# Kernel optimization log

Measured on AMD Instinct MI355X. Metric: run time of the kernel, lower is better.

The kernel has to match this reference:

```python
import jax, jax.numpy as jnp
import numpy as np

N = 100000   # nodes (single ntype)
E = 1600000  # edges per relation
R = 3        # relations
IN, H, OUT = 128, 128, 64


def setup_inputs() -> dict:
    key = jax.random.key(0)
    ks = jax.random.split(key, 6)
    x = jax.random.normal(ks[0], (N, IN), jnp.float32)
    W1 = jax.random.normal(ks[1], (R, IN, H), jnp.float32) * 0.05
    b1 = jax.random.normal(ks[2], (R, H), jnp.float32) * 0.05
    W2 = jax.random.normal(ks[3], (R, H, OUT), jnp.float32) * 0.05
    b2 = jax.random.normal(ks[4], (R, OUT), jnp.float32) * 0.05
    # edge_index[l, r, 0] = src ids, edge_index[l, r, 1] = dst ids for layer l, relation r
    edge_index = jax.random.randint(ks[5], (2, R, 2, E), 0, N, jnp.int32)
    return {"x": x, "W1": W1, "b1": b1, "W2": W2, "b2": b2, "edge_index": edge_index}


def _graph_conv(h, src, dst, W, b, n):
    """DGL GraphConv with norm='both': D_dst^{-1/2} A D_src^{-1/2} h W + b.
    Degrees are clamped to min 1 as in DGL."""
    ones = jnp.ones(src.shape[0], h.dtype)
    deg_out = jnp.clip(jax.ops.segment_sum(ones, src, num_segments=n), 1.0)
    deg_in = jnp.clip(jax.ops.segment_sum(ones, dst, num_segments=n), 1.0)
    m = (h * jax.lax.rsqrt(deg_out)[:, None])[src]          # [E, d] gather
    agg = jax.ops.segment_sum(m, dst, num_segments=n)       # [N, d] scatter-add
    return (agg * jax.lax.rsqrt(deg_in)[:, None]) @ W + b


def _hetero_layer(h, edges, W, b):
    # HeteroGraphConv default aggregate='sum' over relations sharing a dst ntype
    n = h.shape[0]
    out = _graph_conv(h, edges[0, 0], edges[0, 1], W[0], b[0], n)
    for r in range(1, edges.shape[0]):
        out = out + _graph_conv(h, edges[r, 0], edges[r, 1], W[r], b[r], n)
    return out


def reference(x, W1, b1, W2, b2, edge_index):
    h = jax.nn.relu(_hetero_layer(x, edge_index[0], W1, b1))  # dropout = identity (eval)
    return _hetero_layer(h, edge_index[1], W2, b2)
```

## Files before the change

kernel.cpp:

```cpp
#include <hip/hip_runtime.h>

#define N_NODES 100000
#define N_EDGES 1600000
#define NBUCK 250
#define BSZ 400
#define CHUNK 8192
#define NCHUNK 196
#define CAP 8192
#define MTILES 6250
#define NTILE 13
#define NKEY (BSZ * NTILE)
#define NKEYP 5376

typedef _Float16 half8 __attribute__((ext_vector_type(8)));
typedef _Float16 half2v __attribute__((ext_vector_type(2)));
typedef float floatx4 __attribute__((ext_vector_type(4)));

#define OFF_DEG   0ull
#define OFF_GC    4800000ull
#define OFF_BB    4806144ull
#define OFF_BC    4812288ull
#define OFF_RS    4818432ull
#define OFF_START 9618432ull
#define OFF_PAIRS 12018432ull
#define OFF_XH    50418432ull
#define OFF_W1F   76018432ull
#define OFF_W2F   76116736ull
#define OFF_AGG   76165888ull
#define OFF_HW    152965888ull

#define OFF_DDS   OFF_AGG
#define OFF_GCS   (OFF_AGG + 19200000ull)
#define OFF_BBS   (OFF_AGG + 19206144ull)
#define OFF_BCS   (OFF_AGG + 19212288ull)

__device__ __forceinline__ void lds_scan256(int* a) {
    int t = threadIdx.x;
    for (int off = 1; off < 256; off <<= 1) {
        int v = (t >= off) ? a[t - off] : 0;
        __syncthreads();
        a[t] += v;
        __syncthreads();
    }
}

__global__ __launch_bounds__(256) void k_bhist2(const int* __restrict__ ei,
                                                int* __restrict__ gcount_d,
                                                int* __restrict__ gcount_s) {
    int lr = blockIdx.y;
    int e0 = blockIdx.x * CHUNK;
    int n = min(CHUNK, N_EDGES - e0);
    const int* bs = ei + (size_t)lr * 2 * N_EDGES + e0;
    const int* bd = bs + N_EDGES;
    __shared__ int lhs[256];
    __shared__ int lhd[256];
    int t = threadIdx.x;
    lhs[t] = 0; lhd[t] = 0;
    __syncthreads();
    for (int i = t; i < n; i += 256) {
        atomicAdd(&lhs[bs[i] / BSZ], 1);
        atomicAdd(&lhd[bd[i] / BSZ], 1);
    }
    __syncthreads();
    if (t < NBUCK) {
        if (lhd[t]) atomicAdd(&gcount_d[lr * NBUCK + t], lhd[t]);
        if (lhs[t]) atomicAdd(&gcount_s[lr * NBUCK + t], lhs[t]);
    }
}

__global__ __launch_bounds__(256) void k_bscan(const int* __restrict__ gcount,
                                               int* __restrict__ bbase,
                                               int* __restrict__ bcursor) {
    int lr = blockIdx.x, t = threadIdx.x;
    __shared__ int a[256];
    int v = (t < NBUCK) ? gcount[lr * NBUCK + t] : 0;
    a[t] = v;
    __syncthreads();
    lds_scan256(a);
    if (t < NBUCK) {
        int excl = a[t] - v;
        bbase[lr * NBUCK + t] = excl;
        bcursor[lr * NBUCK + t] = excl;
    }
}

__global__ __launch_bounds__(256) void k_bpart(const int* __restrict__ ei,
                                               int* __restrict__ bcursor,
                                               int* __restrict__ pairs) {
    int lr = blockIdx.y;
    int e0 = blockIdx.x * CHUNK;
    int n = min(CHUNK, N_EDGES - e0);
    const int* bs = ei + (size_t)lr * 2 * N_EDGES + e0;
    const int* bd = bs + N_EDGES;
    __shared__ int lh[256];
    __shared__ int lexcl[256];
    __shared__ int lcur[256];
    __shared__ int gb[256];
    __shared__ int staged[CHUNK];
    __shared__ unsigned char stb[CHUNK];
    int t = threadIdx.x;
    lh[t] = 0;
    __syncthreads();
    for (int i = t; i < n; i += 256)
        atomicAdd(&lh[bd[i] / BSZ], 1);
    __syncthreads();
    int cnt_t = lh[t];
    __syncthreads();
    lds_scan256(lh);
    int excl_t = lh[t] - cnt_t;
    lexcl[t] = excl_t;
    lcur[t] = excl_t;
    if (t < NBUCK) gb[t] = cnt_t ? atomicAdd(&bcursor[lr * NBUCK + t], cnt_t) : 0;
    __syncthreads();
    for (int i = t; i < n; i += 256) {
        int s = bs[i], d = bd[i];
        int b = d / BSZ;
        int dd = d - b * BSZ;
        int p = atomicAdd(&lcur[b], 1);
        staged[p] = s | (dd << 17);
        stb[p] = (unsigned char)b;
    }
    __syncthreads();
    int* outp = pairs + (size_t)lr * N_EDGES;
    for (int i = t; i < n; i += 256) {
        int b = stb[i];
        outp[gb[b] + (i - lexcl[b])] = staged[i];
    }
}

__global__ __launch_bounds__(256) void k_bpart_s(const int* __restrict__ ei,
                                                 int* __restrict__ bcursor_s,
                                                 short* __restrict__ dds) {
    int lr = blockIdx.y;
    int e0 = blockIdx.x * CHUNK;
    int n = min(CHUNK, N_EDGES - e0);
    const int* bs = ei + (size_t)lr * 2 * N_EDGES + e0;
    __shared__ int lh[256];
    __shared__ int lexcl[256];
    __shared__ int lcur[256];
    __shared__ int gb[256];
    __shared__ short staged[CHUNK];
    __shared__ unsigned char stb[CHUNK];
    int t = threadIdx.x;
    lh[t] = 0;
    __syncthreads();
    for (int i = t; i < n; i += 256)
        atomicAdd(&lh[bs[i] / BSZ], 1);
    __syncthreads();
    int cnt_t = lh[t];
    __syncthreads();
    lds_scan256(lh);
    int excl_t = lh[t] - cnt_t;
    lexcl[t] = excl_t;
    lcur[t] = excl_t;
    if (t < NBUCK) gb[t] = cnt_t ? atomicAdd(&bcursor_s[lr * NBUCK + t], cnt_t) : 0;
    __syncthreads();
    for (int i = t; i < n; i += 256) {
        int s = bs[i];
        int b = s / BSZ;
        int p = atomicAdd(&lcur[b], 1);
        staged[p] = (short)(s - b * BSZ);
        stb[p] = (unsigned char)b;
    }
    __syncthreads();
    short* outp = dds + (size_t)lr * N_EDGES;
    for (int i = t; i < n; i += 256) {
        int b = stb[i];
        outp[gb[b] + (i - lexcl[b])] = staged[i];
    }
}

__global__ __launch_bounds__(256) void k_bcount_s(const int* __restrict__ bbase_s,
                                                  const short* __restrict__ dds,
                                                  int* __restrict__ deg) {
    int lr = blockIdx.y, b = blockIdx.x;
    int layer = lr / 3, r = lr % 3;
    int base = bbase_s[lr * NBUCK + b];
    int next = (b < NBUCK - 1) ? bbase_s[lr * NBUCK + b + 1] : N_EDGES;
    int cnt = next - base;
    const short* reg = dds + (size_t)lr * N_EDGES + base;
    __shared__ int h[BSZ];
    int t = threadIdx.x;
    h[t] = 0;
    if (t < BSZ - 256) h[t + 256] = 0;
    __syncthreads();
    for (int i = t; i < cnt; i += 256)
        atomicAdd(&h[reg[i]], 1);
    __syncthreads();
    int* degout = deg + (size_t)layer * 6 * N_NODES + (size_t)r * N_NODES + b * BSZ;
    degout[t] = h[t];
    if (t < BSZ - 256) degout[t + 256] = h[t + 256];
}

__global__ __launch_bounds__(256) void k_bsort(const int* __restrict__ bbase,
                                               int* __restrict__ pairs,
                                               int* __restrict__ start,
                                               int* __restrict__ deg) {
    int lr = blockIdx.y, b = blockIdx.x;
    int layer = lr / 3, r = lr % 3;
    int base = bbase[lr * NBUCK + b];
    int next = (b < NBUCK - 1) ? bbase[lr * NBUCK + b + 1] : N_EDGES;
    int cnt = next - base;
    int* reg = pairs + (size_t)lr * N_EDGES + base;
    __shared__ int staged[CAP];
    __shared__ int hist[NKEYP];
    __shared__ int tsum[256];
    int t = threadIdx.x;
    for (int i = t; i < NKEYP; i += 256) hist[i] = 0;
    __syncthreads();
    for (int i = t; i < cnt; i += 256) {
        int v = reg[i];
        if (i < CAP) staged[i] = v;
        int key = (v >> 17) * NTILE + ((v & 0x1FFFF) >> 13);
        atomicAdd(&hist[key], 1);
    }
    __syncthreads();
    int b0 = t * 21;
    int loc[21];
    int s = 0;
#pragma unroll
    for (int k = 0; k < 21; k++) { loc[k] = s; s += hist[b0 + k]; }
    tsum[t] = s;
    __syncthreads();
    lds_scan256(tsum);
    int tbase = tsum[t] - s;
#pragma unroll
    for (int k = 0; k < 21; k++) hist[b0 + k] = tbase + loc[k];
    __syncthreads();
    int d0 = b * BSZ;
    {
        int st = hist[t * NTILE];
        int en = hist[(t + 1) * NTILE];
        start[(size_t)lr * N_NODES + d0 + t] = base + st;
        deg[(size_t)layer * 6 * N_NODES + (size_t)(3 + r) * N_NODES + d0 + t] = en - st;
        if (t < BSZ - 256) {
            int t2 = t + 256;
            int st2 = hist[t2 * NTILE];
            int en2 = hist[(t2 + 1) * NTILE];
            start[(size_t)lr * N_NODES + d0 + t2] = base + st2;
            deg[(size_t)layer * 6 * N_NODES + (size_t)(3 + r) * N_NODES + d0 + t2] = en2 - st2;
        }
    }
    __syncthreads();
    for (int i = t; i < cnt; i += 256) {
        int v = (i < CAP) ? staged[i] : reg[i];
        int key = (v >> 17) * NTILE + ((v & 0x1FFFF) >> 13);
        int p = atomicAdd(&hist[key], 1);
        reg[p] = v & 0x1FFFF;
    }
}

__global__ __launch_bounds__(256) void k_rsqrt(const int* __restrict__ deg,
                                               float* __restrict__ rs) {
    int i = blockIdx.x * 256 + threadIdx.x;
    if (i >= 12 * N_NODES) return;
    int v = deg[i];
    rs[i] = rsqrtf((float)(v < 1 ? 1 : v));
}

__global__ __launch_bounds__(256) void k_cvt_x(const float* __restrict__ x,
                                               _Float16* __restrict__ xh) {
    int i = blockIdx.x * 256 + threadIdx.x;
    if (i >= N_NODES * 64) return;
    float2 v = ((const float2*)x)[i];
    half2v h; h.x = (_Float16)v.x; h.y = (_Float16)v.y;
    ((half2v*)xh)[i] = h;
}

__global__ __launch_bounds__(256) void k_repack(const float* __restrict__ W1,
                                                const float* __restrict__ W2,
                                                _Float16* __restrict__ W1f,
                                                _Float16* __restrict__ W2f) {
    int i = blockIdx.x * 256 + threadIdx.x;
    if (i < 96 * 512) {
        int g = i >> 9, rem = i & 511, L = rem >> 3, j = rem & 7;
        int kc = g >> 3, nt = g & 7;
        int k = kc * 32 + (L >> 4) * 8 + j;
        int n = nt * 16 + (L & 15);
        W1f[i] = (_Float16)W1[k * 128 + n];
    } else if (i < 96 * 512 + 48 * 512) {
        int ii = i - 96 * 512;
        int g = ii >> 9, rem = ii & 511, L = rem >> 3, j = rem & 7;
        int kc = g / 12, nt = g % 12;
        int k = kc * 32 + (L >> 4) * 8 + j;
        int n = nt * 16 + (L & 15);
        int r = n >> 6, c = n & 63;
        W2f[ii] = (_Float16)W2[r * 8192 + k * 64 + c];
    }
}

__device__ __forceinline__ void accum_rel1(const int* __restrict__ sorted, int j, int n,
                                           const float* __restrict__ rsrow,
                                           const half2v* __restrict__ x2,
                                           int lane, float2& acc) {
    for (int base = 0; base < n; base += 64) {
        int c = n - base; if (c > 64) c = 64;
        int s_l = (lane < c) ? sorted[j + base + lane] : 0;
        float w_l = (lane < c) ? rsrow[s_l] : 0.f;
        int q = 0;
        for (; q + 8 <= c; q += 8) {
            int ss[8]; float ww[8]; half2v vv[8];
#pragma unroll
            for (int u = 0; u < 8; u++) { ss[u] = __shfl(s_l, q + u); ww[u] = __shfl(w_l, q + u); }
#pragma unroll
            for (int u = 0; u < 8; u++) vv[u] = x2[(size_t)ss[u] * 64 + lane];
#pragma unroll
            for (int u = 0; u < 8; u++) {
                acc.x += ww[u] * (float)vv[u].x;
                acc.y += ww[u] * (float)vv[u].y;
            }
        }
        for (; q < c; q++) {
            int s = __shfl(s_l, q); float w = __shfl(w_l, q);
            half2v v = x2[(size_t)s * 64 + lane];
            acc.x += w * (float)v.x; acc.y += w * (float)v.y;
        }
    }
}

__global__ __launch_bounds__(256) void k_pull1(const int* __restrict__ sorted,
                                               const int* __restrict__ start,
                                               const int* __restrict__ deg,
                                               const float* __restrict__ rs,
                                               const _Float16* __restrict__ xh,
                                               _Float16* __restrict__ agg) {
    int wid = threadIdx.x >> 6, lane = threadIdx.x & 63;
    int dst = blockIdx.x * 4 + wid;
    if (dst >= N_NODES) return;
    const half2v* x2 = (const half2v*)xh;
    const int* deg0in = deg + 3 * N_NODES;
    float2 a0 = make_float2(0.f, 0.f), a1 = a0, a2 = a0;
    accum_rel1(sorted, start[dst], deg0in[dst], rs, x2, lane, a0);
    accum_rel1(sorted + N_EDGES, start[N_NODES + dst], deg0in[N_NODES + dst],
               rs + N_NODES, x2, lane, a1);
    accum_rel1(sorted + 2 * N_EDGES, start[2 * N_NODES + dst], deg0in[2 * N_NODES + dst],
               rs + 2 * N_NODES, x2, lane, a2);
    size_t mbase = (size_t)(dst >> 4) * 48 * 128;
    int moff = (dst & 15) * 8;
#pragma unroll
    for (int r = 0; r < 3; r++) {
        float2 a = (r == 0) ? a0 : (r == 1) ? a1 : a2;
        float w = rs[(size_t)(3 + r) * N_NODES + dst];
        int k = r * 128 + 2 * lane;
        size_t idx = mbase + (size_t)(k >> 3) * 128 + moff + (k & 7);
        half2v h; h.x = (_Float16)(a.x * w); h.y = (_Float16)(a.y * w);
        *(half2v*)(agg + idx) = h;
    }
}

__global__ __launch_bounds__(256) void k_gemm12(const _Float16* __restrict__ Af,
                                                const _Float16* __restrict__ W1f,
                                                const float* __restrict__ b1,
                                                const _Float16* __restrict__ W2f,
                                                const float* __restrict__ rs1out,
                                                _Float16* __restrict__ hW) {
    __shared__ _Float16 Hs[4][2048];
    int tid = threadIdx.x;
    int w = tid >> 6, L = tid & 63;
    int mt = blockIdx.x * 4 + w;
    if (mt >= MTILES) return;
    const half8* A8 = (const half8*)Af;
    const half8* B1 = (const half8*)W1f;
    const half8* B2 = (const half8*)W2f;

    floatx4 acc[8];
#pragma unroll
    for (int nt = 0; nt < 8; nt++) acc[nt] = (floatx4)(0.f);
#pragma unroll
    for (int kc = 0; kc < 12; kc++) {
        half8 a = A8[(size_t)mt * 768 + kc * 64 + L];
#pragma unroll
        for (int nt = 0; nt < 8; nt++) {
            half8 b = B1[(kc * 8 + nt) * 64 + L];
            acc[nt] = __builtin_amdgcn_mfma_f32_16x16x32_f16(a, b, acc[nt], 0, 0, 0);
        }
    }
    int cl = L & 15, rw = L >> 4;
#pragma unroll
    for (int nt = 0; nt < 8; nt++) {
        int n = nt * 16 + cl;
        float bs = b1[n] + b1[128 + n] + b1[256 + n];
#pragma unroll
        for (int j = 0; j < 4; j++) {
            int mm = rw * 4 + j;
            float v = acc[nt][j] + bs;
            v = v > 0.f ? v : 0.f;
            Hs[w][(n >> 3) * 128 + mm * 8 + (n & 7)] = (_Float16)v;
        }
    }
    __syncthreads();

    const half8* H8 = (const half8*)(&Hs[w][0]);
    floatx4 acc2[12];
#pragma unroll
    for (int nt = 0; nt < 12; nt++) acc2[nt] = (floatx4)(0.f);
#pragma unroll
    for (int kc = 0; kc < 4; kc++) {
        half8 a = H8[kc * 64 + L];
#pragma unroll
        for (int nt = 0; nt < 12; nt++) {
            half8 b = B2[(kc * 12 + nt) * 64 + L];
            acc2[nt] = __builtin_amdgcn_mfma_f32_16x16x32_f16(a, b, acc2[nt], 0, 0, 0);
        }
    }
#pragma unroll
    for (int j = 0; j < 4; j++) {
        int mm = mt * 16 + rw * 4 + j;
        float wr[3] = {rs1out[mm], rs1out[N_NODES + mm], rs1out[2 * N_NODES + mm]};
#pragma unroll
        for (int nt = 0; nt < 12; nt++) {
            int n = nt * 16 + cl;
            hW[(size_t)mm * 192 + n] = (_Float16)(acc2[nt][j] * wr[nt >> 2]);
        }
    }
}

__device__ __forceinline__ void accum_rel2(const int* __restrict__ sorted, int j, int n,
                                           const _Float16* __restrict__ hWr,
                                           int lane, float& acc) {
    for (int base = 0; base < n; base += 64) {
        int c = n - base; if (c > 64) c = 64;
        int s_l = (lane < c) ? sorted[j + base + lane] : 0;
        int q = 0;
        for (; q + 8 <= c; q += 8) {
            int ss[8]; _Float16 vv[8];
#pragma unroll
            for (int u = 0; u < 8; u++) ss[u] = __shfl(s_l, q + u);
#pragma unroll
            for (int u = 0; u < 8; u++) vv[u] = hWr[(size_t)ss[u] * 192 + lane];
#pragma unroll
            for (int u = 0; u < 8; u++) acc += (float)vv[u];
        }
        for (; q < c; q++) {
            int s = __shfl(s_l, q);
            acc += (float)hWr[(size_t)s * 192 + lane];
        }
    }
}

__global__ __launch_bounds__(256) void k_pull2(const int* __restrict__ sorted1,
                                               const int* __restrict__ start1,
                                               const int* __restrict__ deg1,
                                               const float* __restrict__ rs1,
                                               const _Float16* __restrict__ hW,
                                               const float* __restrict__ b2,
                                               float* __restrict__ out) {
    int wid = threadIdx.x >> 6, lane = threadIdx.x & 63;
    int dst = blockIdx.x * 4 + wid;
    if (dst >= N_NODES) return;
    const int* deg1in = deg1 + 3 * N_NODES;
    float a0 = 0.f, a1 = 0.f, a2 = 0.f;
    accum_rel2(sorted1, start1[dst], deg1in[dst], hW, lane, a0);
    accum_rel2(sorted1 + N_EDGES, start1[N_NODES + dst], deg1in[N_NODES + dst],
               hW + 64, lane, a1);
    accum_rel2(sorted1 + 2 * N_EDGES, start1[2 * N_NODES + dst], deg1in[2 * N_NODES + dst],
               hW + 128, lane, a2);
    float o = a0 * rs1[3 * N_NODES + dst] + a1 * rs1[4 * N_NODES + dst] +
              a2 * rs1[5 * N_NODES + dst] + b2[lane] + b2[64 + lane] + b2[128 + lane];
    out[(size_t)dst * 64 + lane] = o;
}

extern "C" void kernel_launch(void* const* d_in, const int* in_sizes, int n_in,
                              void* d_out, int out_size, void* d_ws, size_t ws_size,
                              hipStream_t stream) {
    (void)in_sizes; (void)n_in; (void)out_size; (void)ws_size;
    const float* x  = (const float*)d_in[0];
    const float* W1 = (const float*)d_in[1];
    const float* b1 = (const float*)d_in[2];
    const float* W2 = (const float*)d_in[3];
    const float* b2 = (const float*)d_in[4];
    const int*   ei = (const int*)d_in[5];
    float* out = (float*)d_out;

    char* ws = (char*)d_ws;
    int*      deg     = (int*)(ws + OFF_DEG);
    int*      gcount  = (int*)(ws + OFF_GC);
    int*      bbase   = (int*)(ws + OFF_BB);
    int*      bcursor = (int*)(ws + OFF_BC);
    float*    rs      = (float*)(ws + OFF_RS);
    int*      start   = (int*)(ws + OFF_START);
    int*      pairs   = (int*)(ws + OFF_PAIRS);
    _Float16* xh      = (_Float16*)(ws + OFF_XH);
    _Float16* W1f     = (_Float16*)(ws + OFF_W1F);
    _Float16* W2f     = (_Float16*)(ws + OFF_W2F);
    _Float16* agg     = (_Float16*)(ws + OFF_AGG);
    _Float16* hW      = (_Float16*)(ws + OFF_HW);
    short*    dds     = (short*)(ws + OFF_DDS);
    int*      gcount_s= (int*)(ws + OFF_GCS);
    int*      bbase_s = (int*)(ws + OFF_BBS);
    int*      bcursor_s=(int*)(ws + OFF_BCS);

    hipMemsetAsync(gcount, 0, 6144, stream);
    hipMemsetAsync(gcount_s, 0, 6144, stream);

    k_cvt_x<<<25000, 256, 0, stream>>>(x, xh);
    k_repack<<<288, 256, 0, stream>>>(W1, W2, W1f, W2f);
    k_bhist2<<<dim3(NCHUNK, 6), 256, 0, stream>>>(ei, gcount, gcount_s);
    k_bscan<<<6, 256, 0, stream>>>(gcount, bbase, bcursor);
    k_bscan<<<6, 256, 0, stream>>>(gcount_s, bbase_s, bcursor_s);
    k_bpart<<<dim3(NCHUNK, 6), 256, 0, stream>>>(ei, bcursor, pairs);
    k_bpart_s<<<dim3(NCHUNK, 6), 256, 0, stream>>>(ei, bcursor_s, dds);
    k_bsort<<<dim3(NBUCK, 6), 256, 0, stream>>>(bbase, pairs, start, deg);
    k_bcount_s<<<dim3(NBUCK, 6), 256, 0, stream>>>(bbase_s, dds, deg);
    k_rsqrt<<<4688, 256, 0, stream>>>(deg, rs);
    k_pull1<<<25000, 256, 0, stream>>>(pairs, start, deg, rs, xh, agg);
    k_gemm12<<<(MTILES + 3) / 4, 256, 0, stream>>>(agg, W1f, b1, W2f,
                                                   rs + 6 * (size_t)N_NODES, hW);
    k_pull2<<<25000, 256, 0, stream>>>(pairs + 3 * (size_t)N_EDGES,
                                       start + 3 * (size_t)N_NODES,
                                       deg + 6 * (size_t)N_NODES,
                                       rs + 6 * (size_t)N_NODES,
                                       hW, b2, out);
}
```

Before: 768.4 us.

## Reuse chunk histograms in partitioning, split pull kernels by feature half and relation

The histogram kernel now stores per-chunk bucket counts, so the two partition kernels skip recounting destination and source buckets. The two scans are merged into one launch. The layer-1 pull is split across two grid halves that each gather 64 feature columns. hW is stored as three per-relation planes of 64 columns, and the layer-2 pull runs one grid slice per relation, adding its partial sum into a zeroed output with atomics. This trades recounting work for extra histogram traffic, and gives up wide half2 gathers for narrower, more numerous blocks plus a memset and float atomics on the output.

```diff
diff --git a/kernel.cpp b/kernel.cpp
--- a/kernel.cpp
+++ b/kernel.cpp
@@ -33,6 +33,8 @@
 #define OFF_GCS   (OFF_AGG + 19200000ull)
 #define OFF_BBS   (OFF_AGG + 19206144ull)
 #define OFF_BCS   (OFF_AGG + 19212288ull)
+#define OFF_CHD   (OFF_AGG + 19218432ull)
+#define OFF_CHS   (OFF_AGG + 20422656ull)
 
 __device__ __forceinline__ void lds_scan256(int* a) {
     int t = threadIdx.x;
@@ -46,9 +48,12 @@
 
 __global__ __launch_bounds__(256) void k_bhist2(const int* __restrict__ ei,
                                                 int* __restrict__ gcount_d,
-                                                int* __restrict__ gcount_s) {
+                                                int* __restrict__ gcount_s,
+                                                int* __restrict__ chd,
+                                                int* __restrict__ chs) {
     int lr = blockIdx.y;
-    int e0 = blockIdx.x * CHUNK;
+    int cx = blockIdx.x;
+    int e0 = cx * CHUNK;
     int n = min(CHUNK, N_EDGES - e0);
     const int* bs = ei + (size_t)lr * 2 * N_EDGES + e0;
     const int* bd = bs + N_EDGES;
@@ -62,33 +67,44 @@
         atomicAdd(&lhd[bd[i] / BSZ], 1);
     }
     __syncthreads();
+    chd[(lr * NCHUNK + cx) * 256 + t] = lhd[t];
+    chs[(lr * NCHUNK + cx) * 256 + t] = lhs[t];
     if (t < NBUCK) {
         if (lhd[t]) atomicAdd(&gcount_d[lr * NBUCK + t], lhd[t]);
         if (lhs[t]) atomicAdd(&gcount_s[lr * NBUCK + t], lhs[t]);
     }
 }
 
-__global__ __launch_bounds__(256) void k_bscan(const int* __restrict__ gcount,
-                                               int* __restrict__ bbase,
-                                               int* __restrict__ bcursor) {
-    int lr = blockIdx.x, t = threadIdx.x;
+__global__ __launch_bounds__(256) void k_bscan2(const int* __restrict__ gc_d,
+                                                const int* __restrict__ gc_s,
+                                                int* __restrict__ bb_d,
+                                                int* __restrict__ bc_d,
+                                                int* __restrict__ bb_s,
+                                                int* __restrict__ bc_s) {
+    int q = blockIdx.x, t = threadIdx.x;
+    int lr = (q < 6) ? q : q - 6;
+    const int* gc = (q < 6) ? gc_d : gc_s;
+    int* bb = (q < 6) ? bb_d : bb_s;
+    int* bc = (q < 6) ? bc_d : bc_s;
     __shared__ int a[256];
-    int v = (t < NBUCK) ? gcount[lr * NBUCK + t] : 0;
+    int v = (t < NBUCK) ? gc[lr * NBUCK + t] : 0;
     a[t] = v;
     __syncthreads();
     lds_scan256(a);
     if (t < NBUCK) {
         int excl = a[t] - v;
-        bbase[lr * NBUCK + t] = excl;
-        bcursor[lr * NBUCK + t] = excl;
+        bb[lr * NBUCK + t] = excl;
+        bc[lr * NBUCK + t] = excl;
     }
 }
 
 __global__ __launch_bounds__(256) void k_bpart(const int* __restrict__ ei,
+                                               const int* __restrict__ chd,
                                                int* __restrict__ bcursor,
                                                int* __restrict__ pairs) {
     int lr = blockIdx.y;
-    int e0 = blockIdx.x * CHUNK;
+    int cx = blockIdx.x;
+    int e0 = cx * CHUNK;
     int n = min(CHUNK, N_EDGES - e0);
     const int* bs = ei + (size_t)lr * 2 * N_EDGES + e0;
     const int* bd = bs + N_EDGES;
@@ -99,12 +115,8 @@
     __shared__ int staged[CHUNK];
     __shared__ unsigned char stb[CHUNK];
     int t = threadIdx.x;
-    lh[t] = 0;
-    __syncthreads();
-    for (int i = t; i < n; i += 256)
-        atomicAdd(&lh[bd[i] / BSZ], 1);
-    __syncthreads();
-    int cnt_t = lh[t];
+    int cnt_t = chd[(lr * NCHUNK + cx) * 256 + t];
+    lh[t] = cnt_t;
     __syncthreads();
     lds_scan256(lh);
     int excl_t = lh[t] - cnt_t;
@@ -129,10 +141,12 @@
 }
 
 __global__ __launch_bounds__(256) void k_bpart_s(const int* __restrict__ ei,
+                                                 const int* __restrict__ chs,
                                                  int* __restrict__ bcursor_s,
                                                  short* __restrict__ dds) {
     int lr = blockIdx.y;
-    int e0 = blockIdx.x * CHUNK;
+    int cx = blockIdx.x;
+    int e0 = cx * CHUNK;
     int n = min(CHUNK, N_EDGES - e0);
     const int* bs = ei + (size_t)lr * 2 * N_EDGES + e0;
     __shared__ int lh[256];
@@ -142,12 +156,8 @@
     __shared__ short staged[CHUNK];
     __shared__ unsigned char stb[CHUNK];
     int t = threadIdx.x;
-    lh[t] = 0;
-    __syncthreads();
-    for (int i = t; i < n; i += 256)
-        atomicAdd(&lh[bs[i] / BSZ], 1);
-    __syncthreads();
-    int cnt_t = lh[t];
+    int cnt_t = chs[(lr * NCHUNK + cx) * 256 + t];
+    lh[t] = cnt_t;
     __syncthreads();
     lds_scan256(lh);
     int excl_t = lh[t] - cnt_t;
@@ -289,31 +299,27 @@
     }
 }
 
-__device__ __forceinline__ void accum_rel1(const int* __restrict__ sorted, int j, int n,
-                                           const float* __restrict__ rsrow,
-                                           const half2v* __restrict__ x2,
-                                           int lane, float2& acc) {
+__device__ __forceinline__ void accum1(const int* __restrict__ sorted, int j, int n,
+                                       const float* __restrict__ rsrow,
+                                       const _Float16* __restrict__ xcol,
+                                       int lane, float& acc) {
     for (int base = 0; base < n; base += 64) {
         int c = n - base; if (c > 64) c = 64;
         int s_l = (lane < c) ? sorted[j + base + lane] : 0;
         float w_l = (lane < c) ? rsrow[s_l] : 0.f;
         int q = 0;
         for (; q + 8 <= c; q += 8) {
-            int ss[8]; float ww[8]; half2v vv[8];
+            int ss[8]; float ww[8]; _Float16 vv[8];
 #pragma unroll
             for (int u = 0; u < 8; u++) { ss[u] = __shfl(s_l, q + u); ww[u] = __shfl(w_l, q + u); }
 #pragma unroll
-            for (int u = 0; u < 8; u++) vv[u] = x2[(size_t)ss[u] * 64 + lane];
-#pragma unroll
-            for (int u = 0; u < 8; u++) {
-                acc.x += ww[u] * (float)vv[u].x;
-                acc.y += ww[u] * (float)vv[u].y;
-            }
+            for (int u = 0; u < 8; u++) vv[u] = xcol[(size_t)ss[u] * 128];
+#pragma unroll
+            for (int u = 0; u < 8; u++) acc += ww[u] * (float)vv[u];
         }
         for (; q < c; q++) {
             int s = __shfl(s_l, q); float w = __shfl(w_l, q);
-            half2v v = x2[(size_t)s * 64 + lane];
-            acc.x += w * (float)v.x; acc.y += w * (float)v.y;
+            acc += w * (float)xcol[(size_t)s * 128];
         }
     }
 }
@@ -327,24 +333,24 @@
     int wid = threadIdx.x >> 6, lane = threadIdx.x & 63;
     int dst = blockIdx.x * 4 + wid;
     if (dst >= N_NODES) return;
-    const half2v* x2 = (const half2v*)xh;
+    int p = blockIdx.y;
+    const _Float16* xcol = xh + p * 64 + lane;
     const int* deg0in = deg + 3 * N_NODES;
-    float2 a0 = make_float2(0.f, 0.f), a1 = a0, a2 = a0;
-    accum_rel1(sorted, start[dst], deg0in[dst], rs, x2, lane, a0);
-    accum_rel1(sorted + N_EDGES, start[N_NODES + dst], deg0in[N_NODES + dst],
-               rs + N_NODES, x2, lane, a1);
-    accum_rel1(sorted + 2 * N_EDGES, start[2 * N_NODES + dst], deg0in[2 * N_NODES + dst],
-               rs + 2 * N_NODES, x2, lane, a2);
+    float a0 = 0.f, a1 = 0.f, a2 = 0.f;
+    accum1(sorted, start[dst], deg0in[dst], rs, xcol, lane, a0);
+    accum1(sorted + N_EDGES, start[N_NODES + dst], deg0in[N_NODES + dst],
+           rs + N_NODES, xcol, lane, a1);
+    accum1(sorted + 2 * N_EDGES, start[2 * N_NODES + dst], deg0in[2 * N_NODES + dst],
+           rs + 2 * N_NODES, xcol, lane, a2);
     size_t mbase = (size_t)(dst >> 4) * 48 * 128;
     int moff = (dst & 15) * 8;
 #pragma unroll
     for (int r = 0; r < 3; r++) {
-        float2 a = (r == 0) ? a0 : (r == 1) ? a1 : a2;
+        float a = (r == 0) ? a0 : (r == 1) ? a1 : a2;
         float w = rs[(size_t)(3 + r) * N_NODES + dst];
-        int k = r * 128 + 2 * lane;
+        int k = r * 128 + p * 64 + lane;
         size_t idx = mbase + (size_t)(k >> 3) * 128 + moff + (k & 7);
-        half2v h; h.x = (_Float16)(a.x * w); h.y = (_Float16)(a.y * w);
-        *(half2v*)(agg + idx) = h;
+        agg[idx] = (_Float16)(a * w);
     }
 }
 
@@ -410,14 +416,16 @@
 #pragma unroll
         for (int nt = 0; nt < 12; nt++) {
             int n = nt * 16 + cl;
-            hW[(size_t)mm * 192 + n] = (_Float16)(acc2[nt][j] * wr[nt >> 2]);
-        }
-    }
-}
-
-__device__ __forceinline__ void accum_rel2(const int* __restrict__ sorted, int j, int n,
-                                           const _Float16* __restrict__ hWr,
-                                           int lane, float& acc) {
+            int rel = nt >> 2, c = n & 63;
+            hW[(size_t)rel * (N_NODES * 64) + (size_t)mm * 64 + c] =
+                (_Float16)(acc2[nt][j] * wr[rel]);
+        }
+    }
+}
+
+__device__ __forceinline__ void accum2(const int* __restrict__ sorted, int j, int n,
+                                       const _Float16* __restrict__ hcol,
+                                       int lane, float& acc) {
     for (int base = 0; base < n; base += 64) {
         int c = n - base; if (c > 64) c = 64;
         int s_l = (lane < c) ? sorted[j + base + lane] : 0;
@@ -427,13 +435,13 @@
 #pragma unroll
             for (int u = 0; u < 8; u++) ss[u] = __shfl(s_l, q + u);
 #pragma unroll
-            for (int u = 0; u < 8; u++) vv[u] = hWr[(size_t)ss[u] * 192 + lane];
+            for (int u = 0; u < 8; u++) vv[u] = hcol[(size_t)ss[u] * 64];
 #pragma unroll
             for (int u = 0; u < 8; u++) acc += (float)vv[u];
         }
         for (; q < c; q++) {
             int s = __shfl(s_l, q);
-            acc += (float)hWr[(size_t)s * 192 + lane];
+            acc += (float)hcol[(size_t)s * 64];
         }
     }
 }
@@ -448,16 +456,16 @@
     int wid = threadIdx.x >> 6, lane = threadIdx.x & 63;
     int dst = blockIdx.x * 4 + wid;
     if (dst >= N_NODES) return;
+    int rel = blockIdx.y;
     const int* deg1in = deg1 + 3 * N_NODES;
-    float a0 = 0.f, a1 = 0.f, a2 = 0.f;
-    accum_rel2(sorted1, start1[dst], deg1in[dst], hW, lane, a0);
-    accum_rel2(sorted1 + N_EDGES, start1[N_NODES + dst], deg1in[N_NODES + dst],
-               hW + 64, lane, a1);
-    accum_rel2(sorted1 + 2 * N_EDGES, start1[2 * N_NODES + dst], deg1in[2 * N_NODES + dst],
-               hW + 128, lane, a2);
-    float o = a0 * rs1[3 * N_NODES + dst] + a1 * rs1[4 * N_NODES + dst] +
-              a2 * rs1[5 * N_NODES + dst] + b2[lane] + b2[64 + lane] + b2[128 + lane];
-    out[(size_t)dst * 64 + lane] = o;
+    const _Float16* hcol = hW + (size_t)rel * (N_NODES * 64) + lane;
+    float acc = 0.f;
+    accum2(sorted1 + (size_t)rel * N_EDGES,
+           start1[(size_t)rel * N_NODES + dst],
+           deg1in[(size_t)rel * N_NODES + dst], hcol, lane, acc);
+    float v = acc * rs1[(size_t)(3 + rel) * N_NODES + dst];
+    if (rel == 0) v += b2[lane] + b2[64 + lane] + b2[128 + lane];
+    atomicAdd(&out[(size_t)dst * 64 + lane], v);
 }
 
 extern "C" void kernel_launch(void* const* d_in, const int* in_sizes, int n_in,
@@ -489,26 +497,28 @@
     int*      gcount_s= (int*)(ws + OFF_GCS);
     int*      bbase_s = (int*)(ws + OFF_BBS);
     int*      bcursor_s=(int*)(ws + OFF_BCS);
+    int*      chd     = (int*)(ws + OFF_CHD);
+    int*      chs     = (int*)(ws + OFF_CHS);
 
     hipMemsetAsync(gcount, 0, 6144, stream);
     hipMemsetAsync(gcount_s, 0, 6144, stream);
+    hipMemsetAsync(out, 0, (size_t)N_NODES * 64 * 4, stream);
 
     k_cvt_x<<<25000, 256, 0, stream>>>(x, xh);
     k_repack<<<288, 256, 0, stream>>>(W1, W2, W1f, W2f);
-    k_bhist2<<<dim3(NCHUNK, 6), 256, 0, stream>>>(ei, gcount, gcount_s);
-    k_bscan<<<6, 256, 0, stream>>>(gcount, bbase, bcursor);
-    k_bscan<<<6, 256, 0, stream>>>(gcount_s, bbase_s, bcursor_s);
-    k_bpart<<<dim3(NCHUNK, 6), 256, 0, stream>>>(ei, bcursor, pairs);
-    k_bpart_s<<<dim3(NCHUNK, 6), 256, 0, stream>>>(ei, bcursor_s, dds);
+    k_bhist2<<<dim3(NCHUNK, 6), 256, 0, stream>>>(ei, gcount, gcount_s, chd, chs);
+    k_bscan2<<<12, 256, 0, stream>>>(gcount, gcount_s, bbase, bcursor, bbase_s, bcursor_s);
+    k_bpart<<<dim3(NCHUNK, 6), 256, 0, stream>>>(ei, chd, bcursor, pairs);
+    k_bpart_s<<<dim3(NCHUNK, 6), 256, 0, stream>>>(ei, chs, bcursor_s, dds);
     k_bsort<<<dim3(NBUCK, 6), 256, 0, stream>>>(bbase, pairs, start, deg);
     k_bcount_s<<<dim3(NBUCK, 6), 256, 0, stream>>>(bbase_s, dds, deg);
     k_rsqrt<<<4688, 256, 0, stream>>>(deg, rs);
-    k_pull1<<<25000, 256, 0, stream>>>(pairs, start, deg, rs, xh, agg);
+    k_pull1<<<dim3(25000, 2), 256, 0, stream>>>(pairs, start, deg, rs, xh, agg);
     k_gemm12<<<(MTILES + 3) / 4, 256, 0, stream>>>(agg, W1f, b1, W2f,
                                                    rs + 6 * (size_t)N_NODES, hW);
-    k_pull2<<<25000, 256, 0, stream>>>(pairs + 3 * (size_t)N_EDGES,
-                                       start + 3 * (size_t)N_NODES,
-                                       deg + 6 * (size_t)N_NODES,
-                                       rs + 6 * (size_t)N_NODES,
-                                       hW, b2, out);
-}
+    k_pull2<<<dim3(25000, 3), 256, 0, stream>>>(pairs + 3 * (size_t)N_EDGES,
+                                                start + 3 * (size_t)N_NODES,
+                                                deg + 6 * (size_t)N_NODES,
+                                                rs + 6 * (size_t)N_NODES,
+                                                hW, b2, out);
+}
```

After: 897.1 us. 1.17x slower.
